# Kernel tuning notes

Hardware: AMD Instinct MI355X
Metric: run time of the kernel (lower is better)

Reference implementation:

```python
import jax, jax.numpy as jnp
import numpy as np
import math

INPUT_SIZE = 1024
B, L1, L2 = 8, 2048, 2048


def setup_inputs() -> dict:
    key = jax.random.key(0)
    ks = jax.random.split(key, 10)
    s = 1.0 / math.sqrt(INPUT_SIZE)
    return {
        "Q": jax.random.normal(ks[0], (B, L1, INPUT_SIZE), dtype=jnp.float32),
        "K": jax.random.normal(ks[1], (B, L2, INPUT_SIZE), dtype=jnp.float32),
        "V": jax.random.normal(ks[2], (B, L2, INPUT_SIZE), dtype=jnp.float32),
        "K_mask": jax.random.randint(ks[3], (B, L2), 0, 2, dtype=jnp.int32),
        "Wq": jax.random.normal(ks[4], (INPUT_SIZE, INPUT_SIZE), dtype=jnp.float32) * s,
        "bq": jax.random.normal(ks[5], (INPUT_SIZE,), dtype=jnp.float32) * s,
        "Wk": jax.random.normal(ks[6], (INPUT_SIZE, INPUT_SIZE), dtype=jnp.float32) * s,
        "bk": jax.random.normal(ks[7], (INPUT_SIZE,), dtype=jnp.float32) * s,
        "Wv": jax.random.normal(ks[8], (INPUT_SIZE, INPUT_SIZE), dtype=jnp.float32) * s,
        "bv": jax.random.normal(ks[9], (INPUT_SIZE,), dtype=jnp.float32) * s,
    }


def reference(Q, K, V, K_mask, Wq, bq, Wk, bk, Wv, bv):
    # Linear projections (torch Linear: x @ W.T + b)
    q = jnp.einsum('bld,ed->ble', Q, Wq) + bq
    k = jnp.einsum('bld,ed->ble', K, Wk) + bk
    v = jnp.einsum('bld,ed->ble', V, Wv) + bv
    # scores: [B, L1, L2], scaled by sqrt(input_size)
    scores = jnp.einsum('bqd,bkd->bqk', q, k) / math.sqrt(INPUT_SIZE)
    # K_mask == 1 marks padding -> -inf before softmax
    scores = jnp.where(K_mask[:, None, :] == 1, -jnp.inf, scores)
    alpha = jax.nn.softmax(scores, axis=-1)
    matched_seq = jnp.einsum('bqk,bkd->bqd', alpha, v)
    return matched_seq
```

## Files before the change

### kernel.cpp

```cpp
#include <hip/hip_runtime.h>


using u16 = unsigned short;
using frag_ab = __attribute__((ext_vector_type(8))) short;
using frag_cd = __attribute__((ext_vector_type(4))) float;

#define BAR() asm volatile("s_barrier" ::: "memory")
#define WAITV(n) asm volatile("s_waitcnt vmcnt(" #n ")" ::: "memory")
#define L(d, ab, h) (lds + (((d) * 4) + ((ab) * 2) + (h)) * 8192)

__device__ __forceinline__ u16 f2bf(float f) {
  union { float f; unsigned u; } c; c.f = f;
  unsigned u = c.u;
  return (u16)((u + 0x7FFFu + ((u >> 16) & 1u)) >> 16);
}

__device__ __forceinline__ void async_ld16(const void* g, void* l) {
  __builtin_amdgcn_global_load_lds(
      (const __attribute__((address_space(1))) unsigned*)g,
      (__attribute__((address_space(3))) unsigned*)l, 16, 0, 0);
}

__global__ void cvt_f32_bf16(const float* __restrict__ in, u16* __restrict__ out, long n) {
  long i = ((long)blockIdx.x * 256 + threadIdx.x) * 4;
  if (i >= n) return;
  float4 v = *reinterpret_cast<const float4*>(in + i);
  ushort4 o = make_ushort4(f2bf(v.x), f2bf(v.y), f2bf(v.z), f2bf(v.w));
  *reinterpret_cast<ushort4*>(out + i) = o;
}

__device__ __forceinline__ void stage_half(const u16* __restrict__ g_rowbase,
                                           long Kstr, u16* l_half,
                                           int wave, int lane) {
  const int t = wave * 64 + lane;
  #pragma unroll
  for (int i = 0; i < 2; i++) {
    const int row = i * 64 + (t >> 3);
    const int cb  = (t & 7) * 16;
    const int cbs = cb ^ ((row & 7) << 4);
    async_ld16(g_rowbase + (long)row * Kstr + (cbs >> 1),
               l_half + i * 4096 + wave * 512);
  }
}

__device__ __forceinline__ frag_ab ld_frag(const u16* half_base, int r, int k) {
  const int idx = r * 64 + (k ^ ((r & 7) << 3));
  return *reinterpret_cast<const frag_ab*>(half_base + idx);
}

template<int OUT_MODE>
__device__ __forceinline__ void
gemm256_body(const u16* __restrict__ A, const u16* __restrict__ Bt,
             void* __restrict__ Cout, const float* __restrict__ bias,
             int M, int N, int K, long sA, long sB, long sC, float scale,
             u16* lds)
{
  const int gx = gridDim.x, gy = gridDim.y, gz = gridDim.z;
  const int nwg = gx * gy * gz;
  const int lin = ((int)blockIdx.z * gy + blockIdx.y) * gx + blockIdx.x;
  const int q8 = nwg >> 3, r8 = nwg & 7;
  const int xcd = lin & 7, idx8 = lin >> 3;
  const int swz = (xcd < r8 ? xcd * (q8 + 1) : r8 * (q8 + 1) + (xcd - r8) * q8) + idx8;
  const int z = swz / (gx * gy);
  const int rem = swz % (gx * gy);
  const int m0 = (rem / gx) * 256;
  const int n0 = (rem % gx) * 256;

  const u16* Ab = A + (long)z * sA;
  const u16* Bb = Bt + (long)z * sB;

  const int tid = threadIdx.x;
  const int wave = tid >> 6, lane = tid & 63;
  const int wm = wave >> 2;
  const int wn = wave & 3;
  const int ln15 = lane & 15, kof = (lane >> 4) * 8;
  const int rB0 = (wn & 1) * 64;
  const int NT = K >> 6;

  frag_cd acc[8][4];
  #pragma unroll
  for (int i = 0; i < 8; i++)
    #pragma unroll
    for (int j = 0; j < 4; j++)
      acc[i][j] = (frag_cd){0.f, 0.f, 0.f, 0.f};

  stage_half(Ab + (long)(m0 +   0) * K, K, L(0, 0, 0), wave, lane);
  stage_half(Ab + (long)(m0 + 128) * K, K, L(0, 0, 1), wave, lane);
  stage_half(Bb + (long)(n0 +   0) * K, K, L(0, 1, 0), wave, lane);
  stage_half(Bb + (long)(n0 + 128) * K, K, L(0, 1, 1), wave, lane);
  {
    const int ts = (1 < NT) ? 1 : NT - 1;
    stage_half(Ab + (long)(m0 +   0) * K + ts * 64, K, L(1, 0, 0), wave, lane);
    stage_half(Ab + (long)(m0 + 128) * K + ts * 64, K, L(1, 0, 1), wave, lane);
  }
  WAITV(4);
  BAR();

  for (int t = 0; t < NT; ++t) {
    const int d = t & 1;
    const u16* Al = L(d, 0, wm);
    const u16* Bl = L(d, 1, wn >> 1);
    const int tb = (t + 1 < NT) ? t + 1 : NT - 1;
    const int ta = (t + 2 < NT) ? t + 2 : NT - 1;

    frag_ab bf[4][2], af[8][2];

    #pragma unroll
    for (int bn = 0; bn < 4; ++bn)
      #pragma unroll
      for (int kk = 0; kk < 2; ++kk)
        bf[bn][kk] = ld_frag(Bl, rB0 + bn * 16 + ln15, kk * 32 + kof);
    #pragma unroll
    for (int am = 0; am < 2; ++am)
      #pragma unroll
      for (int kk = 0; kk < 2; ++kk)
        af[am][kk] = ld_frag(Al, am * 16 + ln15, kk * 32 + kof);
    stage_half(Bb + (long)(n0 + 0) * K + tb * 64, K, L(d ^ 1, 1, 0), wave, lane);
    BAR();
    __builtin_amdgcn_s_setprio(1);
    #pragma unroll
    for (int am = 0; am < 2; ++am)
      #pragma unroll
      for (int bn = 0; bn < 4; ++bn)
        #pragma unroll
        for (int kk = 0; kk < 2; ++kk)
          acc[am][bn] = __builtin_amdgcn_mfma_f32_16x16x32_bf16(af[am][kk], bf[bn][kk], acc[am][bn], 0, 0, 0);
    __builtin_amdgcn_s_setprio(0);
    BAR();

    #pragma unroll
    for (int am = 2; am < 8; ++am)
      #pragma unroll
      for (int kk = 0; kk < 2; ++kk)
        af[am][kk] = ld_frag(Al, am * 16 + ln15, kk * 32 + kof);
    stage_half(Bb + (long)(n0 + 128) * K + tb * 64, K, L(d ^ 1, 1, 1), wave, lane);
    BAR();
    __builtin_amdgcn_s_setprio(1);
    #pragma unroll
    for (int am = 2; am < 4; ++am)
      #pragma unroll
      for (int bn = 0; bn < 4; ++bn)
        #pragma unroll
        for (int kk = 0; kk < 2; ++kk)
          acc[am][bn] = __builtin_amdgcn_mfma_f32_16x16x32_bf16(af[am][kk], bf[bn][kk], acc[am][bn], 0, 0, 0);
    __builtin_amdgcn_s_setprio(0);
    BAR();

    stage_half(Ab + (long)(m0 + 0) * K + ta * 64, K, L(d, 0, 0), wave, lane);
    BAR();
    __builtin_amdgcn_s_setprio(1);
    #pragma unroll
    for (int am = 4; am < 6; ++am)
      #pragma unroll
      for (int bn = 0; bn < 4; ++bn)
        #pragma unroll
        for (int kk = 0; kk < 2; ++kk)
          acc[am][bn] = __builtin_amdgcn_mfma_f32_16x16x32_bf16(af[am][kk], bf[bn][kk], acc[am][bn], 0, 0, 0);
    __builtin_amdgcn_s_setprio(0);
    BAR();

    stage_half(Ab + (long)(m0 + 128) * K + ta * 64, K, L(d, 0, 1), wave, lane);
    BAR();
    __builtin_amdgcn_s_setprio(1);
    #pragma unroll
    for (int am = 6; am < 8; ++am)
      #pragma unroll
      for (int bn = 0; bn < 4; ++bn)
        #pragma unroll
        for (int kk = 0; kk < 2; ++kk)
          acc[am][bn] = __builtin_amdgcn_mfma_f32_16x16x32_bf16(af[am][kk], bf[bn][kk], acc[am][bn], 0, 0, 0);
    __builtin_amdgcn_s_setprio(0);
    WAITV(4);
    BAR();
  }

  WAITV(0);
  BAR();

  const int cl = lane & 15;
  const int rb = (lane >> 4) * 4;
  #pragma unroll
  for (int bn = 0; bn < 4; ++bn) {
    const int gcol = n0 + wn * 64 + bn * 16 + cl;
    const float badd = bias ? bias[gcol] : 0.f;
    #pragma unroll
    for (int am = 0; am < 8; ++am) {
      #pragma unroll
      for (int r = 0; r < 4; ++r) {
        const int grow = m0 + wm * 128 + am * 16 + rb + r;
        const float val = acc[am][bn][r] * scale + badd;
        if (OUT_MODE == 0) {
          ((float*)Cout)[(long)z * sC + (long)grow * N + gcol] = val;
        } else if (OUT_MODE == 1) {
          ((u16*)Cout)[(long)z * sC + (long)grow * N + gcol] = f2bf(val);
        } else {
          const int bb = grow >> 11, l2 = grow & 2047;
          ((u16*)Cout)[((long)bb * N + gcol) * 2048 + l2] = f2bf(val);
        }
      }
    }
  }
}

__global__ void __launch_bounds__(512, 2)
proj_gemm(const u16* A, const u16* Bt, void* C, const float* bias,
          int M, int N, int K, long sA, long sB, long sC, float scale) {
  __shared__ u16 lds[8 * 8192];
  gemm256_body<1>(A, Bt, C, bias, M, N, K, sA, sB, sC, scale, lds);
}
__global__ void __launch_bounds__(512, 2)
projv_gemm(const u16* A, const u16* Bt, void* C, const float* bias,
           int M, int N, int K, long sA, long sB, long sC, float scale) {
  __shared__ u16 lds[8 * 8192];
  gemm256_body<2>(A, Bt, C, bias, M, N, K, sA, sB, sC, scale, lds);
}
__global__ void __launch_bounds__(512, 2)
qk_gemm(const u16* A, const u16* Bt, void* C, const float* bias,
        int M, int N, int K, long sA, long sB, long sC, float scale) {
  __shared__ u16 lds[8 * 8192];
  gemm256_body<0>(A, Bt, C, bias, M, N, K, sA, sB, sC, scale, lds);
}
__global__ void __launch_bounds__(512, 2)
pv_gemm(const u16* A, const u16* Bt, void* C, const float* bias,
        int M, int N, int K, long sA, long sB, long sC, float scale) {
  __shared__ u16 lds[8 * 8192];
  gemm256_body<0>(A, Bt, C, bias, M, N, K, sA, sB, sC, scale, lds);
}

__global__ void softmax_rows(const float* __restrict__ S, const int* __restrict__ Km,
                             u16* __restrict__ P)
{
  const long row = blockIdx.x;
  const int b = (int)(row >> 11);
  const float* s = S + row * 2048;
  const int* mask = Km + (long)b * 2048;
  u16* p = P + row * 2048;

  const int t = threadIdx.x;
  const int base = t * 8;

  float4 v0 = *reinterpret_cast<const float4*>(s + base);
  float4 v1 = *reinterpret_cast<const float4*>(s + base + 4);
  int4 mA = *reinterpret_cast<const int4*>(mask + base);
  int4 mB = *reinterpret_cast<const int4*>(mask + base + 4);

  float vals[8] = {v0.x, v0.y, v0.z, v0.w, v1.x, v1.y, v1.z, v1.w};
  const int mk[8] = {mA.x, mA.y, mA.z, mA.w, mB.x, mB.y, mB.z, mB.w};

  float mx = -3.0e38f;
  #pragma unroll
  for (int i = 0; i < 8; i++) if (!mk[i]) mx = fmaxf(mx, vals[i]);
  #pragma unroll
  for (int off = 32; off > 0; off >>= 1) mx = fmaxf(mx, __shfl_xor(mx, off));

  __shared__ float redm[4], reds[4];
  const int wave = t >> 6, lane = t & 63;
  if (lane == 0) redm[wave] = mx;
  __syncthreads();
  mx = fmaxf(fmaxf(redm[0], redm[1]), fmaxf(redm[2], redm[3]));

  float e[8]; float sum = 0.f;
  #pragma unroll
  for (int i = 0; i < 8; i++) { e[i] = mk[i] ? 0.f : __expf(vals[i] - mx); sum += e[i]; }
  #pragma unroll
  for (int off = 32; off > 0; off >>= 1) sum += __shfl_xor(sum, off);
  if (lane == 0) reds[wave] = sum;
  __syncthreads();
  sum = reds[0] + reds[1] + reds[2] + reds[3];
  const float inv = 1.f / sum;

  ushort4 o0 = make_ushort4(f2bf(e[0]*inv), f2bf(e[1]*inv), f2bf(e[2]*inv), f2bf(e[3]*inv));
  ushort4 o1 = make_ushort4(f2bf(e[4]*inv), f2bf(e[5]*inv), f2bf(e[6]*inv), f2bf(e[7]*inv));
  *reinterpret_cast<ushort4*>(p + base) = o0;
  *reinterpret_cast<ushort4*>(p + base + 4) = o1;
}

extern "C" void kernel_launch(void* const* d_in, const int* in_sizes, int n_in,
                              void* d_out, int out_size, void* d_ws, size_t ws_size,
                              hipStream_t stream) {
  (void)in_sizes; (void)n_in; (void)out_size;

  const float* Qin  = (const float*)d_in[0];
  const float* Kin  = (const float*)d_in[1];
  const float* Vin  = (const float*)d_in[2];
  const int*   Kmask = (const int*)d_in[3];
  const float* Wq = (const float*)d_in[4];
  const float* bq = (const float*)d_in[5];
  const float* Wk = (const float*)d_in[6];
  const float* bk = (const float*)d_in[7];
  const float* Wv = (const float*)d_in[8];
  const float* bv = (const float*)d_in[9];

  char* ws = (char*)d_ws;
  const size_t MB = 1024UL * 1024UL;
  const long NQKV = 8L * 2048 * 1024;
  const long NW = 1024L * 1024;
  const dim3 blk(256);
  const dim3 gblk(512);
  const float rs = 0.03125f;

  if (ws_size >= 226 * MB) {
    u16*  qb = (u16*)(ws);
    u16*  kb = (u16*)(ws + 32 * MB);
    u16*  vT = (u16*)(ws + 64 * MB);
    u16*  P  = (u16*)(ws + 96 * MB);
    u16*  Xb = (u16*)(ws + 96 * MB);
    float* S = (float*)(ws + 160 * MB);
    u16*  Wb = (u16*)(ws + 224 * MB);

    cvt_f32_bf16<<<dim3(NQKV / 1024), blk, 0, stream>>>(Qin, Xb, NQKV);
    cvt_f32_bf16<<<dim3(NW / 1024), blk, 0, stream>>>(Wq, Wb, NW);
    proj_gemm<<<dim3(4, 64, 1), gblk, 0, stream>>>(Xb, Wb, qb, bq,
        16384, 1024, 1024, 0, 0, 0, 1.f);

    cvt_f32_bf16<<<dim3(NQKV / 1024), blk, 0, stream>>>(Kin, Xb, NQKV);
    cvt_f32_bf16<<<dim3(NW / 1024), blk, 0, stream>>>(Wk, Wb, NW);
    proj_gemm<<<dim3(4, 64, 1), gblk, 0, stream>>>(Xb, Wb, kb, bk,
        16384, 1024, 1024, 0, 0, 0, 1.f);

    cvt_f32_bf16<<<dim3(NQKV / 1024), blk, 0, stream>>>(Vin, Xb, NQKV);
    cvt_f32_bf16<<<dim3(NW / 1024), blk, 0, stream>>>(Wv, Wb, NW);
    projv_gemm<<<dim3(4, 64, 1), gblk, 0, stream>>>(Xb, Wb, vT, bv,
        16384, 1024, 1024, 0, 0, 0, 1.f);

    for (int h = 0; h < 2; h++) {
      const u16* qbH = qb + (long)(4 * h) * 2048 * 1024;
      const u16* kbH = kb + (long)(4 * h) * 2048 * 1024;
      qk_gemm<<<dim3(8, 8, 4), gblk, 0, stream>>>(qbH, kbH, S, nullptr,
          2048, 2048, 1024, 2048L * 1024, 2048L * 1024, 2048L * 2048, rs);
      softmax_rows<<<dim3(8192), blk, 0, stream>>>(
          S, Kmask + (long)(4 * h) * 2048, P + (long)(4 * h) * 2048 * 2048);
    }

    pv_gemm<<<dim3(4, 8, 8), gblk, 0, stream>>>(P, vT, d_out, nullptr,
        2048, 1024, 2048, 2048L * 2048, 1024L * 2048, 2048L * 1024, 1.f);
  } else if (ws_size >= 194 * MB) {
    u16*  qb = (u16*)(ws);
    u16*  kb = (u16*)(ws + 32 * MB);
    u16*  vT = (u16*)(ws + 64 * MB);
    u16*  P  = (u16*)(ws + 96 * MB);
    u16*  Xb = (u16*)(ws + 96 * MB);
    float* S = (float*)(ws + 160 * MB);
    u16*  Wb = (u16*)(ws + 192 * MB);

    cvt_f32_bf16<<<dim3(NQKV / 1024), blk, 0, stream>>>(Qin, Xb, NQKV);
    cvt_f32_bf16<<<dim3(NW / 1024), blk, 0, stream>>>(Wq, Wb, NW);
    proj_gemm<<<dim3(4, 64, 1), gblk, 0, stream>>>(Xb, Wb, qb, bq,
        16384, 1024, 1024, 0, 0, 0, 1.f);

    cvt_f32_bf16<<<dim3(NQKV / 1024), blk, 0, stream>>>(Kin, Xb, NQKV);
    cvt_f32_bf16<<<dim3(NW / 1024), blk, 0, stream>>>(Wk, Wb, NW);
    proj_gemm<<<dim3(4, 64, 1), gblk, 0, stream>>>(Xb, Wb, kb, bk,
        16384, 1024, 1024, 0, 0, 0, 1.f);

    cvt_f32_bf16<<<dim3(NQKV / 1024), blk, 0, stream>>>(Vin, Xb, NQKV);
    cvt_f32_bf16<<<dim3(NW / 1024), blk, 0, stream>>>(Wv, Wb, NW);
    projv_gemm<<<dim3(4, 64, 1), gblk, 0, stream>>>(Xb, Wb, vT, bv,
        16384, 1024, 1024, 0, 0, 0, 1.f);

    for (int p = 0; p < 4; p++) {
      const u16* qbP = qb + (long)(2 * p) * 2048 * 1024;
      const u16* kbP = kb + (long)(2 * p) * 2048 * 1024;
      qk_gemm<<<dim3(8, 8, 2), gblk, 0, stream>>>(qbP, kbP, S, nullptr,
          2048, 2048, 1024, 2048L * 1024, 2048L * 1024, 2048L * 2048, rs);
      softmax_rows<<<dim3(4096), blk, 0, stream>>>(
          S, Kmask + (long)(2 * p) * 2048, P + (long)(2 * p) * 2048 * 2048);
    }

    pv_gemm<<<dim3(4, 8, 8), gblk, 0, stream>>>(P, vT, d_out, nullptr,
        2048, 1024, 2048, 2048L * 2048, 1024L * 2048, 2048L * 1024, 1.f);
  } else {
    u16*  qb = (u16*)(ws);
    u16*  kb = (u16*)(ws + 32 * MB);
    u16*  vT = (u16*)(ws + 64 * MB);
    u16*  Xb = (u16*)(ws + 96 * MB);
    float* S = (float*)(ws + 96 * MB);
    u16*  P  = (u16*)(ws + 112 * MB);
    u16*  Wb = (u16*)(ws + 128 * MB);

    cvt_f32_bf16<<<dim3(NQKV / 1024), blk, 0, stream>>>(Qin, Xb, NQKV);
    cvt_f32_bf16<<<dim3(NW / 1024), blk, 0, stream>>>(Wq, Wb, NW);
    proj_gemm<<<dim3(4, 64, 1), gblk, 0, stream>>>(Xb, Wb, qb, bq,
        16384, 1024, 1024, 0, 0, 0, 1.f);

    cvt_f32_bf16<<<dim3(NQKV / 1024), blk, 0, stream>>>(Kin, Xb, NQKV);
    cvt_f32_bf16<<<dim3(NW / 1024), blk, 0, stream>>>(Wk, Wb, NW);
    proj_gemm<<<dim3(4, 64, 1), gblk, 0, stream>>>(Xb, Wb, kb, bk,
        16384, 1024, 1024, 0, 0, 0, 1.f);

    cvt_f32_bf16<<<dim3(NQKV / 1024), blk, 0, stream>>>(Vin, Xb, NQKV);
    cvt_f32_bf16<<<dim3(NW / 1024), blk, 0, stream>>>(Wv, Wb, NW);
    projv_gemm<<<dim3(4, 64, 1), gblk, 0, stream>>>(Xb, Wb, vT, bv,
        16384, 1024, 1024, 0, 0, 0, 1.f);

    for (int b = 0; b < 8; b++) {
      const u16* qbB = qb + (long)b * 2048 * 1024;
      const u16* kbB = kb + (long)b * 2048 * 1024;
      const u16* vTB = vT + (long)b * 1024 * 2048;
      float* outB = (float*)d_out + (long)b * 2048 * 1024;

      qk_gemm<<<dim3(8, 8, 1), gblk, 0, stream>>>(qbB, kbB, S, nullptr,
          2048, 2048, 1024, 0, 0, 0, rs);
      softmax_rows<<<dim3(2048), blk, 0, stream>>>(S, Kmask + (long)b * 2048, P);
      pv_gemm<<<dim3(4, 8, 1), gblk, 0, stream>>>(P, vTB, outB, nullptr,
          2048, 1024, 2048, 0, 0, 0, 1.f);
    }
  }
}
```

Measured before the change: 388.7 us.

## Reorder GEMM prefetch schedule to prefetch A one tile ahead and B two ahead

Swaps the roles of A and B in the LDS double-buffer prefetch schedule: A tiles are now staged one step ahead into the other buffer, and B tiles two steps ahead into the current buffer after B fragments are consumed. A fragments are loaded incrementally in 2-row groups just before each MFMA block instead of all at once, shrinking the af register array from 8x2 to 2x2. This is meant to lower VGPR pressure and spread LDS reads between compute phases, at the cost of more interleaved LDS loads and barriers, and it changes the correctness conditions of the buffer reuse.

```diff
diff --git a/kernel.cpp b/kernel.cpp
--- a/kernel.cpp
+++ b/kernel.cpp
@@ -89,9 +89,9 @@
   stage_half(Bb + (long)(n0 +   0) * K, K, L(0, 1, 0), wave, lane);
   stage_half(Bb + (long)(n0 + 128) * K, K, L(0, 1, 1), wave, lane);
   {
-    const int ts = (1 < NT) ? 1 : NT - 1;
-    stage_half(Ab + (long)(m0 +   0) * K + ts * 64, K, L(1, 0, 0), wave, lane);
-    stage_half(Ab + (long)(m0 + 128) * K + ts * 64, K, L(1, 0, 1), wave, lane);
+    const int t1 = (1 < NT) ? 1 : 0;
+    stage_half(Bb + (long)(n0 +   0) * K + t1 * 64, K, L(1, 1, 0), wave, lane);
+    stage_half(Bb + (long)(n0 + 128) * K + t1 * 64, K, L(1, 1, 1), wave, lane);
   }
   WAITV(4);
   BAR();
@@ -100,10 +100,10 @@
     const int d = t & 1;
     const u16* Al = L(d, 0, wm);
     const u16* Bl = L(d, 1, wn >> 1);
-    const int tb = (t + 1 < NT) ? t + 1 : NT - 1;
-    const int ta = (t + 2 < NT) ? t + 2 : NT - 1;
-
-    frag_ab bf[4][2], af[8][2];
+    const int tA = (t + 1 < NT) ? t + 1 : NT - 1;
+    const int tB = (t + 2 < NT) ? t + 2 : NT - 1;
+
+    frag_ab bf[4][2], af[2][2];
 
     #pragma unroll
     for (int bn = 0; bn < 4; ++bn)
@@ -115,7 +115,8 @@
       #pragma unroll
       for (int kk = 0; kk < 2; ++kk)
         af[am][kk] = ld_frag(Al, am * 16 + ln15, kk * 32 + kof);
-    stage_half(Bb + (long)(n0 + 0) * K + tb * 64, K, L(d ^ 1, 1, 0), wave, lane);
+    stage_half(Ab + (long)(m0 +   0) * K + tA * 64, K, L(d ^ 1, 0, 0), wave, lane);
+    stage_half(Ab + (long)(m0 + 128) * K + tA * 64, K, L(d ^ 1, 0, 1), wave, lane);
     BAR();
     __builtin_amdgcn_s_setprio(1);
     #pragma unroll
@@ -129,46 +130,55 @@
     BAR();
 
     #pragma unroll
-    for (int am = 2; am < 8; ++am)
+    for (int am = 0; am < 2; ++am)
       #pragma unroll
       for (int kk = 0; kk < 2; ++kk)
-        af[am][kk] = ld_frag(Al, am * 16 + ln15, kk * 32 + kof);
-    stage_half(Bb + (long)(n0 + 128) * K + tb * 64, K, L(d ^ 1, 1, 1), wave, lane);
+        af[am][kk] = ld_frag(Al, (2 + am) * 16 + ln15, kk * 32 + kof);
+    stage_half(Bb + (long)(n0 + 0) * K + tB * 64, K, L(d, 1, 0), wave, lane);
     BAR();
     __builtin_amdgcn_s_setprio(1);
     #pragma unroll
-    for (int am = 2; am < 4; ++am)
+    for (int am = 0; am < 2; ++am)
       #pragma unroll
       for (int bn = 0; bn < 4; ++bn)
         #pragma unroll
         for (int kk = 0; kk < 2; ++kk)
-          acc[am][bn] = __builtin_amdgcn_mfma_f32_16x16x32_bf16(af[am][kk], bf[bn][kk], acc[am][bn], 0, 0, 0);
+          acc[2 + am][bn] = __builtin_amdgcn_mfma_f32_16x16x32_bf16(af[am][kk], bf[bn][kk], acc[2 + am][bn], 0, 0, 0);
     __builtin_amdgcn_s_setprio(0);
     BAR();
 
-    stage_half(Ab + (long)(m0 + 0) * K + ta * 64, K, L(d, 0, 0), wave, lane);
+    #pragma unroll
+    for (int am = 0; am < 2; ++am)
+      #pragma unroll
+      for (int kk = 0; kk < 2; ++kk)
+        af[am][kk] = ld_frag(Al, (4 + am) * 16 + ln15, kk * 32 + kof);
+    stage_half(Bb + (long)(n0 + 128) * K + tB * 64, K, L(d, 1, 1), wave, lane);
     BAR();
     __builtin_amdgcn_s_setprio(1);
     #pragma unroll
-    for (int am = 4; am < 6; ++am)
+    for (int am = 0; am < 2; ++am)
       #pragma unroll
       for (int bn = 0; bn < 4; ++bn)
         #pragma unroll
         for (int kk = 0; kk < 2; ++kk)
-          acc[am][bn] = __builtin_amdgcn_mfma_f32_16x16x32_bf16(af[am][kk], bf[bn][kk], acc[am][bn], 0, 0, 0);
+          acc[4 + am][bn] = __builtin_amdgcn_mfma_f32_16x16x32_bf16(af[am][kk], bf[bn][kk], acc[4 + am][bn], 0, 0, 0);
     __builtin_amdgcn_s_setprio(0);
     BAR();
 
-    stage_half(Ab + (long)(m0 + 128) * K + ta * 64, K, L(d, 0, 1), wave, lane);
+    #pragma unroll
+    for (int am = 0; am < 2; ++am)
+      #pragma unroll
+      for (int kk = 0; kk < 2; ++kk)
+        af[am][kk] = ld_frag(Al, (6 + am) * 16 + ln15, kk * 32 + kof);
     BAR();
     __builtin_amdgcn_s_setprio(1);
     #pragma unroll
-    for (int am = 6; am < 8; ++am)
+    for (int am = 0; am < 2; ++am)
       #pragma unroll
       for (int bn = 0; bn < 4; ++bn)
         #pragma unroll
         for (int kk = 0; kk < 2; ++kk)
-          acc[am][bn] = __builtin_amdgcn_mfma_f32_16x16x32_bf16(af[am][kk], bf[bn][kk], acc[am][bn], 0, 0, 0);
+          acc[6 + am][bn] = __builtin_amdgcn_mfma_f32_16x16x32_bf16(af[am][kk], bf[bn][kk], acc[6 + am][bn], 0, 0, 0);
     __builtin_amdgcn_s_setprio(0);
     WAITV(4);
     BAR();
```

After: 383.1 us. Within noise of the previous version (-1.5%).
